# Kernel optimization log

Hardware: AMD Instinct MI355X
Metric: run time of the kernel (lower is better)

## Reference

```python
import jax, jax.numpy as jnp
import numpy as np
import math


def setup_inputs() -> dict:
    key = jax.random.key(0)
    ks = jax.random.split(key, 7)
    d_input, d_state, d_output = 256, 256, 256
    B_, S_ = 8, 4096
    x = jax.random.normal(ks[0], (B_, S_, d_input), dtype=jnp.float32)
    log_lambda_real = jax.random.normal(ks[1], (d_state,), dtype=jnp.float32)
    lambda_imag = jax.random.normal(ks[2], (d_state,), dtype=jnp.float32)
    dt = jnp.clip(0.01 + jax.random.normal(ks[3], (d_state,), dtype=jnp.float32) * 0.01, 0.005, 0.1)
    log_dt = jnp.log(dt)
    B = jax.random.normal(ks[4], (d_state, d_input), dtype=jnp.float32) / d_state ** 0.5
    C_real = jax.random.normal(ks[5], (d_output, d_state), dtype=jnp.float32) / d_state ** 0.5
    C_imag = jax.random.normal(ks[6], (d_output, d_state), dtype=jnp.float32) / d_state ** 0.5
    return {"x": x, "log_lambda_real": log_lambda_real, "lambda_imag": lambda_imag,
            "log_dt": log_dt, "B": B, "C_real": C_real, "C_imag": C_imag}


def reference(x, log_lambda_real, lambda_imag, log_dt, B, C_real, C_imag):
    batch, seq_len, _ = x.shape
    # continuous-time poles and step sizes
    Lambda = -jnp.exp(log_lambda_real) + 1j * lambda_imag            # [N] complex
    dt = jnp.clip(jnp.exp(log_dt), 0.005, 0.1)                       # [N]
    # bilinear discretization
    denom = 1.0 - 0.5 * dt * Lambda                                  # [N] complex
    A_bar = (1.0 + 0.5 * dt * Lambda) / denom                        # [N] complex
    B_bar = (dt / denom)[:, None] * B                                # [N, d_in] complex
    # project input into state space: u[b,s,n] (complex)
    u = jnp.matmul(x, B_bar.real.T) + 1j * jnp.matmul(x, B_bar.imag.T)  # [B,S,N]
    # kernel A^0 .. A^{L-1} via cumprod (faithful to original)
    A_poles = jnp.broadcast_to(A_bar[:, None], (A_bar.shape[0], seq_len))  # [N,S]
    A_cp = jnp.cumprod(A_poles, axis=1)
    A_powers = jnp.concatenate([jnp.ones_like(A_cp[:, :1]), A_cp[:, :-1]], axis=1)  # [N,S]
    # FFT causal convolution
    n_fft = 2 ** math.ceil(math.log2(seq_len * 2 - 1))
    u_t = jnp.swapaxes(u, 1, 2)                                      # [B,N,S]
    u_f = jnp.fft.fft(u_t, n=n_fft, axis=-1)                          # [B,N,F]
    A_f = jnp.fft.fft(A_powers, n=n_fft, axis=-1)                     # [N,F]
    h = jnp.fft.ifft(u_f * A_f[None], n=n_fft, axis=-1)[..., :seq_len]  # [B,N,S]
    h = jnp.swapaxes(h, 1, 2)                                         # [B,S,N]
    # output projection, keep real part
    C_c = C_real + 1j * C_imag                                        # [d_out,N]
    return jnp.matmul(h, C_c.T).real                                  # [B,S,d_out]
```

## Files before the change

### kernel.cpp

```cpp
#include <hip/hip_runtime.h>
#include <hip/hip_bf16.h>

#define BB 8
#define SS 4096
#define NN 256
#define MM (BB*SS)
#define CHUNK 32
#define NCH (SS/CHUNK)

#define WS_FINR 0
#define WS_FINI (BB*NCH*NN)
#define WS_CARR (2*BB*NCH*NN)
#define WS_CARI (3*BB*NCH*NN)
#define WS_FLOATS (4*BB*NCH*NN)
#define WS_V_BYTE  ((size_t)WS_FLOATS * 4)
#define WS_CP_BYTE (WS_V_BYTE + (size_t)MM*NN*2)

typedef __bf16 bf16_t;
typedef bf16_t bf16x8 __attribute__((ext_vector_type(8)));
typedef float  f32x4  __attribute__((ext_vector_type(4)));
typedef unsigned int u32x4 __attribute__((ext_vector_type(4)));

__device__ inline bf16_t f2b(float f) {
    __hip_bfloat16 h = __float2bfloat16(f);
    return __builtin_bit_cast(bf16_t, h);
}
__device__ inline bf16x8 cvt8(f32x4 a, f32x4 b) {
    bf16x8 o;
    o[0]=f2b(a[0]); o[1]=f2b(a[1]); o[2]=f2b(a[2]); o[3]=f2b(a[3]);
    o[4]=f2b(b[0]); o[5]=f2b(b[1]); o[6]=f2b(b[2]); o[7]=f2b(b[3]);
    return o;
}

__device__ inline void ssm_consts(const float* llr, const float* li, const float* ldt,
                                  int n, float& Ar, float& Ai, float& sr, float& si) {
    float lr = -expf(llr[n]);
    float im = li[n];
    float dt = expf(ldt[n]);
    dt = fminf(fmaxf(dt, 0.005f), 0.1f);
    float hr = 0.5f * dt * lr, hi = 0.5f * dt * im;
    float dr = 1.f - hr, di = -hi;
    float inv = 1.f / (dr*dr + di*di);
    Ar = ((1.f + hr)*dr + hi*di) * inv;
    Ai = (hi*dr - (1.f + hr)*di) * inv;
    sr = dt * dr * inv;
    si = -dt * di * inv;
}

__global__ __launch_bounds__(256) void k1(const float* __restrict__ X,
                                          const float* __restrict__ Bw,
                                          const float* __restrict__ llr,
                                          const float* __restrict__ li,
                                          const float* __restrict__ ldt,
                                          __hip_bfloat16* __restrict__ V,
                                          float* __restrict__ finr,
                                          float* __restrict__ fini) {
    __shared__ bf16x8 lds_a[1024];
    __shared__ bf16x8 lds_b[1024];
    __shared__ __align__(16) __hip_bfloat16 vt[128][128];
    int t = threadIdx.x;
    int w = t >> 6, lane = t & 63;
    int q = lane >> 4, r = lane & 15;
    int Nblk = blockIdx.x;
    int Mblk = blockIdx.y;
    int wmt = (w & 1) * 4;
    int wnt = (w >> 1) * 4;
    f32x4 acc[4][4] = {};

    for (int kk = 0; kk < 4; ++kk) {
        int k0 = kk * 64;
        #pragma unroll
        for (int s = 0; s < 4; ++s) {
            int f    = s * 256 + t;
            int tile = f >> 6;
            int ls   = f & 63;
            int mt   = tile >> 1, kb = tile & 1;
            int qq   = ls >> 4, rr = ls & 15;
            int col  = k0 + kb * 32 + qq * 8;
            const f32x4* pa = (const f32x4*)(X  + (size_t)(Mblk*128 + mt*16 + rr) * 256 + col);
            const f32x4* pb = (const f32x4*)(Bw + (size_t)(Nblk*128 + mt*16 + rr) * 256 + col);
            lds_a[f] = cvt8(pa[0], pa[1]);
            lds_b[f] = cvt8(pb[0], pb[1]);
        }
        __syncthreads();
        #pragma unroll
        for (int kb = 0; kb < 2; ++kb) {
            bf16x8 af[4], bfr[4];
            #pragma unroll
            for (int i = 0; i < 4; ++i) {
                af[i]  = lds_a[((wmt + i)*2 + kb)*64 + lane];
                bfr[i] = lds_b[((wnt + i)*2 + kb)*64 + lane];
            }
            #pragma unroll
            for (int mt = 0; mt < 4; ++mt)
                #pragma unroll
                for (int nt = 0; nt < 4; ++nt)
                    acc[mt][nt] = __builtin_amdgcn_mfma_f32_16x16x32_bf16(
                        af[mt], bfr[nt], acc[mt][nt], 0, 0, 0);
        }
        __syncthreads();
    }
    #pragma unroll
    for (int mt = 0; mt < 4; ++mt)
        #pragma unroll
        for (int nt = 0; nt < 4; ++nt)
            #pragma unroll
            for (int reg = 0; reg < 4; ++reg)
                vt[(wmt+mt)*16 + q*4 + reg][(wnt+nt)*16 + r] =
                    __float2bfloat16(acc[mt][nt][reg]);
    __syncthreads();

    int m0 = Mblk * 128;
    #pragma unroll
    for (int jj = 0; jj < 8; ++jj) {
        int s  = t + 256 * jj;
        int rl = s >> 4, cv = s & 15;
        u32x4 val = *(const u32x4*)&vt[rl][cv*8];
        *(u32x4*)(V + (size_t)(m0 + rl) * NN + Nblk*128 + cv*8) = val;
    }
    int n_loc = t & 127, n = Nblk*128 + n_loc;
    float Ar, Ai, sr, si;
    ssm_consts(llr, li, ldt, n, Ar, Ai, sr, si);
    int b = m0 >> 12, cbase = (m0 & 4095) >> 5;
    #pragma unroll
    for (int half = 0; half < 2; ++half) {
        int ch = (t >> 7) + half*2;
        float hr = 0.f, hi = 0.f;
        #pragma unroll 8
        for (int i = 0; i < CHUNK; ++i) {
            float v = __bfloat162float(vt[ch*32 + i][n_loc]);
            float tr = fmaf(Ar, hr, fmaf(-Ai, hi, sr * v));
            float ti = fmaf(Ar, hi, fmaf( Ai, hr, si * v));
            hr = tr; hi = ti;
        }
        int f = (b * NCH + cbase + ch) * NN + n;
        finr[f] = hr; fini[f] = hi;
    }
}

__global__ __launch_bounds__(256) void k2(const float* __restrict__ llr,
                                          const float* __restrict__ li,
                                          const float* __restrict__ ldt,
                                          const float* __restrict__ Cr,
                                          const float* __restrict__ Ci,
                                          float* __restrict__ wsf,
                                          u32x4* __restrict__ Cpack) {
    int t = threadIdx.x;
    if (blockIdx.x < 8) {
        int n = t, b = blockIdx.x;
        float Ar, Ai, sr_, si_;
        ssm_consts(llr, li, ldt, n, Ar, Ai, sr_, si_);
        float pr = Ar, pi = Ai;
        #pragma unroll
        for (int i = 0; i < 5; ++i) { float tt = pr*pr - pi*pi; pi = 2.f*pr*pi; pr = tt; }
        float cr = 0.f, ci = 0.f;
        #pragma unroll 4
        for (int c = 0; c < NCH; ++c) {
            int f = (b * NCH + c) * NN + n;
            wsf[WS_CARR + f] = cr; wsf[WS_CARI + f] = ci;
            float fr = wsf[WS_FINR + f], fi = wsf[WS_FINI + f];
            float tr = fmaf(pr, cr, fmaf(-pi, ci, fr));
            float ti = fmaf(pr, ci, fmaf( pi, cr, fi));
            cr = tr; ci = ti;
        }
    } else {
        int ks = blockIdx.x - 8;
        const float* src = (ks < 8) ? Cr : Ci;
        float sign = (ks < 8) ? 1.f : -1.f;
        #pragma unroll
        for (int jj = 0; jj < 4; ++jj) {
            int s = t + 256 * jj;
            int ot = s >> 6, lane = s & 63;
            int o  = ot*16 + (lane & 15);
            int kb = (ks & 7)*32 + (lane >> 4)*8;
            bf16x8 v;
            #pragma unroll
            for (int e = 0; e < 8; ++e) v[e] = f2b(sign * src[o*256 + kb + e]);
            Cpack[(ks*16 + ot)*64 + lane] = __builtin_bit_cast(u32x4, v);
        }
    }
}

__global__ __launch_bounds__(512) void k3(const __hip_bfloat16* __restrict__ V,
                                          const float* __restrict__ llr,
                                          const float* __restrict__ li,
                                          const float* __restrict__ ldt,
                                          const float* __restrict__ carr,
                                          const float* __restrict__ cari,
                                          const u32x4* __restrict__ Cpack,
                                          float* __restrict__ out) {
    __shared__ __align__(16) char hlds[65536];
    int t = threadIdx.x;
    int m0 = blockIdx.x * 64;
    int b = m0 >> 12, cbase = (m0 & 4095) >> 5;
    {
        int n = t & 255, ch = t >> 8;
        float Ar, Ai, sr, si;
        ssm_consts(llr, li, ldt, n, Ar, Ai, sr, si);
        int f = (b * NCH + cbase + ch) * NN + n;
        float hr = carr[f], hi = cari[f];
        int oct = n >> 3, j = n & 7;
        const __hip_bfloat16* vp = V + (size_t)(m0 + ch*32) * NN + n;
        #pragma unroll 8
        for (int i = 0; i < CHUNK; ++i) {
            float v = __bfloat162float(vp[i * NN]);
            float tr = fmaf(Ar, hr, fmaf(-Ai, hi, sr * v));
            float ti = fmaf(Ar, hi, fmaf( Ai, hr, si * v));
            hr = tr; hi = ti;
            int ml   = ch*32 + i;
            int octp = oct ^ (ml & 31);
            int off  = ((ml*32 + octp) << 4) + (j << 1);
            *(__hip_bfloat16*)(hlds + off)         = __float2bfloat16(hr);
            *(__hip_bfloat16*)(hlds + 32768 + off) = __float2bfloat16(hi);
        }
    }
    __syncthreads();
    int w = t >> 6, lane = t & 63, q = lane >> 4, r = lane & 15;
    f32x4 acc[4][2] = {};
    #pragma unroll
    for (int ks = 0; ks < 16; ++ks) {
        int base = (ks < 8) ? 0 : 32768;
        int kin  = ks & 7;
        bf16x8 af[4];
        #pragma unroll
        for (int mt = 0; mt < 4; ++mt) {
            int ml   = mt*16 + r;
            int octp = (kin*4 + q) ^ (ml & 31);
            af[mt] = *(const bf16x8*)(hlds + base + ((ml*32 + octp) << 4));
        }
        #pragma unroll
        for (int u = 0; u < 2; ++u) {
            bf16x8 bf_ = __builtin_bit_cast(bf16x8, Cpack[(ks*16 + w*2 + u)*64 + lane]);
            #pragma unroll
            for (int mt = 0; mt < 4; ++mt)
                acc[mt][u] = __builtin_amdgcn_mfma_f32_16x16x32_bf16(
                    af[mt], bf_, acc[mt][u], 0, 0, 0);
        }
    }
    #pragma unroll
    for (int mt = 0; mt < 4; ++mt)
        #pragma unroll
        for (int u = 0; u < 2; ++u)
            #pragma unroll
            for (int reg = 0; reg < 4; ++reg)
                out[(size_t)(m0 + mt*16 + q*4 + reg) * NN + (w*2 + u)*16 + r] =
                    acc[mt][u][reg];
}

extern "C" void kernel_launch(void* const* d_in, const int* in_sizes, int n_in,
                              void* d_out, int out_size, void* d_ws, size_t ws_size,
                              hipStream_t stream) {
    const float* x   = (const float*)d_in[0];
    const float* llr = (const float*)d_in[1];
    const float* li  = (const float*)d_in[2];
    const float* ldt = (const float*)d_in[3];
    const float* Bw  = (const float*)d_in[4];
    const float* Cr  = (const float*)d_in[5];
    const float* Ci  = (const float*)d_in[6];

    float* wsf = (float*)d_ws;
    char*  wsb = (char*)d_ws;
    __hip_bfloat16* V = (__hip_bfloat16*)(wsb + WS_V_BYTE);
    u32x4* Cpack      = (u32x4*)(wsb + WS_CP_BYTE);

    k1<<<dim3(2, 256), 256, 0, stream>>>(x, Bw, llr, li, ldt, V,
                                         wsf + WS_FINR, wsf + WS_FINI);
    k2<<<24, 256, 0, stream>>>(llr, li, ldt, Cr, Ci, wsf, Cpack);
    k3<<<512, 512, 0, stream>>>(V, llr, li, ldt,
                                wsf + WS_CARR, wsf + WS_CARI, Cpack, (float*)d_out);
}
```

Baseline: 138.5 us.

## Fuse carry scan into output kernel and store local chunk states from projection kernel

The projection kernel now computes the chunk-local recurrence itself and writes local real and imaginary states (bf16) instead of the projected input. The sequential cross-chunk carry kernel is removed: each output block recomputes its carry by scanning the prior chunk finals and adds the carry times powers of A to the stored local states. The C packing moves into extra blocks of the first kernel, so there are two launches instead of three. This drops a serial kernel and a launch, but doubles the intermediate bf16 traffic, makes later blocks do a longer redundant carry scan (up to 128 steps), and adds bf16 rounding when local and carry states are summed.

Measured after the change: 135.2 us. 2.4% less time.

```diff
diff --git a/kernel.cpp b/kernel.cpp
--- a/kernel.cpp
+++ b/kernel.cpp
@@ -8,13 +8,11 @@
 #define CHUNK 32
 #define NCH (SS/CHUNK)
 
-#define WS_FINR 0
-#define WS_FINI (BB*NCH*NN)
-#define WS_CARR (2*BB*NCH*NN)
-#define WS_CARI (3*BB*NCH*NN)
-#define WS_FLOATS (4*BB*NCH*NN)
-#define WS_V_BYTE  ((size_t)WS_FLOATS * 4)
-#define WS_CP_BYTE (WS_V_BYTE + (size_t)MM*NN*2)
+#define WS_FINR_B  ((size_t)0)
+#define WS_FINI_B  ((size_t)1  << 20)
+#define WS_HLR_B   ((size_t)2  << 20)
+#define WS_HLI_B   ((size_t)18 << 20)
+#define WS_CP_B    ((size_t)34 << 20)
 
 typedef __bf16 bf16_t;
 typedef bf16_t bf16x8 __attribute__((ext_vector_type(8)));
@@ -24,6 +22,21 @@
 __device__ inline bf16_t f2b(float f) {
     __hip_bfloat16 h = __float2bfloat16(f);
     return __builtin_bit_cast(bf16_t, h);
+}
+__device__ inline float b2f(bf16_t v) {
+    unsigned u = (unsigned)__builtin_bit_cast(unsigned short, v) << 16;
+    return __builtin_bit_cast(float, u);
+}
+__device__ inline float b2f_lo(unsigned v) {
+    unsigned u = v << 16; return __builtin_bit_cast(float, u);
+}
+__device__ inline float b2f_hi(unsigned v) {
+    unsigned u = v & 0xffff0000u; return __builtin_bit_cast(float, u);
+}
+__device__ inline unsigned pack2(float lo, float hi) {
+    unsigned a = (unsigned)__builtin_bit_cast(unsigned short, f2b(lo));
+    unsigned b = (unsigned)__builtin_bit_cast(unsigned short, f2b(hi));
+    return a | (b << 16);
 }
 __device__ inline bf16x8 cvt8(f32x4 a, f32x4 b) {
     bf16x8 o;
@@ -47,22 +60,47 @@
     si = -dt * di * inv;
 }
 
-__global__ __launch_bounds__(256) void k1(const float* __restrict__ X,
-                                          const float* __restrict__ Bw,
-                                          const float* __restrict__ llr,
-                                          const float* __restrict__ li,
-                                          const float* __restrict__ ldt,
-                                          __hip_bfloat16* __restrict__ V,
-                                          float* __restrict__ finr,
-                                          float* __restrict__ fini) {
-    __shared__ bf16x8 lds_a[1024];
-    __shared__ bf16x8 lds_b[1024];
-    __shared__ __align__(16) __hip_bfloat16 vt[128][128];
+__global__ __launch_bounds__(256, 2) void k1(const float* __restrict__ X,
+                                             const float* __restrict__ Bw,
+                                             const float* __restrict__ llr,
+                                             const float* __restrict__ li,
+                                             const float* __restrict__ ldt,
+                                             const float* __restrict__ Cr,
+                                             const float* __restrict__ Ci,
+                                             __hip_bfloat16* __restrict__ HLR,
+                                             __hip_bfloat16* __restrict__ HLI,
+                                             float* __restrict__ finr,
+                                             float* __restrict__ fini,
+                                             u32x4* __restrict__ Cpack) {
+    __shared__ __align__(16) char smem[65536];
+    bf16x8* lds_a = (bf16x8*)smem;
+    bf16x8* lds_b = (bf16x8*)(smem + 16384);
+    __hip_bfloat16 (*vt)[128]  = (__hip_bfloat16(*)[128])(smem + 32768);
+    __hip_bfloat16 (*hit)[128] = (__hip_bfloat16(*)[128])smem;
+
     int t = threadIdx.x;
+    int bid = blockIdx.x;
+    if (bid >= 512) {
+        int ks = bid - 512;
+        const float* src = (ks < 8) ? Cr : Ci;
+        float sign = (ks < 8) ? 1.f : -1.f;
+        #pragma unroll
+        for (int jj = 0; jj < 4; ++jj) {
+            int s = t + 256 * jj;
+            int ot = s >> 6, lane = s & 63;
+            int o  = ot*16 + (lane & 15);
+            int kb = (ks & 7)*32 + (lane >> 4)*8;
+            bf16x8 v;
+            #pragma unroll
+            for (int e = 0; e < 8; ++e) v[e] = f2b(sign * src[o*256 + kb + e]);
+            Cpack[(ks*16 + ot)*64 + lane] = __builtin_bit_cast(u32x4, v);
+        }
+        return;
+    }
+
     int w = t >> 6, lane = t & 63;
     int q = lane >> 4, r = lane & 15;
-    int Nblk = blockIdx.x;
-    int Mblk = blockIdx.y;
+    int Nblk = bid & 1, Mblk = bid >> 1;
     int wmt = (w & 1) * 4;
     int wnt = (w >> 1) * 4;
     f32x4 acc[4][4] = {};
@@ -111,108 +149,109 @@
     __syncthreads();
 
     int m0 = Mblk * 128;
+    int b = m0 >> 12, cbase = (m0 & 4095) >> 5;
+    {
+        int p = t & 63, ch = t >> 6;
+        int n0 = Nblk*128 + p*2;
+        float Ar0,Ai0,sr0,si0, Ar1,Ai1,sr1,si1;
+        ssm_consts(llr, li, ldt, n0,   Ar0, Ai0, sr0, si0);
+        ssm_consts(llr, li, ldt, n0+1, Ar1, Ai1, sr1, si1);
+        float hr0=0.f, hi0=0.f, hr1=0.f, hi1=0.f;
+        #pragma unroll 8
+        for (int i = 0; i < CHUNK; ++i) {
+            int row = ch*32 + i;
+            unsigned vv = *(unsigned*)&vt[row][p*2];
+            float v0 = b2f_lo(vv), v1 = b2f_hi(vv);
+            float t0r = fmaf(Ar0, hr0, fmaf(-Ai0, hi0, sr0 * v0));
+            float t0i = fmaf(Ar0, hi0, fmaf( Ai0, hr0, si0 * v0));
+            float t1r = fmaf(Ar1, hr1, fmaf(-Ai1, hi1, sr1 * v1));
+            float t1i = fmaf(Ar1, hi1, fmaf( Ai1, hr1, si1 * v1));
+            hr0=t0r; hi0=t0i; hr1=t1r; hi1=t1i;
+            *(unsigned*)&vt[row][p*2]  = pack2(hr0, hr1);
+            *(unsigned*)&hit[row][p*2] = pack2(hi0, hi1);
+        }
+        int f = (b * NCH + cbase + ch) * NN + n0;
+        finr[f] = hr0; finr[f+1] = hr1;
+        fini[f] = hi0; fini[f+1] = hi1;
+    }
+    __syncthreads();
     #pragma unroll
     for (int jj = 0; jj < 8; ++jj) {
         int s  = t + 256 * jj;
         int rl = s >> 4, cv = s & 15;
-        u32x4 val = *(const u32x4*)&vt[rl][cv*8];
-        *(u32x4*)(V + (size_t)(m0 + rl) * NN + Nblk*128 + cv*8) = val;
-    }
-    int n_loc = t & 127, n = Nblk*128 + n_loc;
-    float Ar, Ai, sr, si;
-    ssm_consts(llr, li, ldt, n, Ar, Ai, sr, si);
-    int b = m0 >> 12, cbase = (m0 & 4095) >> 5;
-    #pragma unroll
-    for (int half = 0; half < 2; ++half) {
-        int ch = (t >> 7) + half*2;
-        float hr = 0.f, hi = 0.f;
-        #pragma unroll 8
-        for (int i = 0; i < CHUNK; ++i) {
-            float v = __bfloat162float(vt[ch*32 + i][n_loc]);
-            float tr = fmaf(Ar, hr, fmaf(-Ai, hi, sr * v));
-            float ti = fmaf(Ar, hi, fmaf( Ai, hr, si * v));
-            hr = tr; hi = ti;
-        }
-        int f = (b * NCH + cbase + ch) * NN + n;
-        finr[f] = hr; fini[f] = hi;
-    }
-}
-
-__global__ __launch_bounds__(256) void k2(const float* __restrict__ llr,
-                                          const float* __restrict__ li,
-                                          const float* __restrict__ ldt,
-                                          const float* __restrict__ Cr,
-                                          const float* __restrict__ Ci,
-                                          float* __restrict__ wsf,
-                                          u32x4* __restrict__ Cpack) {
-    int t = threadIdx.x;
-    if (blockIdx.x < 8) {
-        int n = t, b = blockIdx.x;
-        float Ar, Ai, sr_, si_;
-        ssm_consts(llr, li, ldt, n, Ar, Ai, sr_, si_);
-        float pr = Ar, pi = Ai;
-        #pragma unroll
-        for (int i = 0; i < 5; ++i) { float tt = pr*pr - pi*pi; pi = 2.f*pr*pi; pr = tt; }
-        float cr = 0.f, ci = 0.f;
-        #pragma unroll 4
-        for (int c = 0; c < NCH; ++c) {
-            int f = (b * NCH + c) * NN + n;
-            wsf[WS_CARR + f] = cr; wsf[WS_CARI + f] = ci;
-            float fr = wsf[WS_FINR + f], fi = wsf[WS_FINI + f];
-            float tr = fmaf(pr, cr, fmaf(-pi, ci, fr));
-            float ti = fmaf(pr, ci, fmaf( pi, cr, fi));
-            cr = tr; ci = ti;
-        }
-    } else {
-        int ks = blockIdx.x - 8;
-        const float* src = (ks < 8) ? Cr : Ci;
-        float sign = (ks < 8) ? 1.f : -1.f;
-        #pragma unroll
-        for (int jj = 0; jj < 4; ++jj) {
-            int s = t + 256 * jj;
-            int ot = s >> 6, lane = s & 63;
-            int o  = ot*16 + (lane & 15);
-            int kb = (ks & 7)*32 + (lane >> 4)*8;
-            bf16x8 v;
-            #pragma unroll
-            for (int e = 0; e < 8; ++e) v[e] = f2b(sign * src[o*256 + kb + e]);
-            Cpack[(ks*16 + ot)*64 + lane] = __builtin_bit_cast(u32x4, v);
-        }
-    }
-}
-
-__global__ __launch_bounds__(512) void k3(const __hip_bfloat16* __restrict__ V,
-                                          const float* __restrict__ llr,
-                                          const float* __restrict__ li,
-                                          const float* __restrict__ ldt,
-                                          const float* __restrict__ carr,
-                                          const float* __restrict__ cari,
-                                          const u32x4* __restrict__ Cpack,
-                                          float* __restrict__ out) {
+        *(u32x4*)(HLR + (size_t)(m0 + rl) * NN + Nblk*128 + cv*8) = *(const u32x4*)&vt[rl][cv*8];
+        *(u32x4*)(HLI + (size_t)(m0 + rl) * NN + Nblk*128 + cv*8) = *(const u32x4*)&hit[rl][cv*8];
+    }
+}
+
+__global__ __launch_bounds__(512, 4) void k3(const __hip_bfloat16* __restrict__ HLR,
+                                             const __hip_bfloat16* __restrict__ HLI,
+                                             const float* __restrict__ finr,
+                                             const float* __restrict__ fini,
+                                             const float* __restrict__ llr,
+                                             const float* __restrict__ li,
+                                             const float* __restrict__ ldt,
+                                             const u32x4* __restrict__ Cpack,
+                                             float* __restrict__ out) {
     __shared__ __align__(16) char hlds[65536];
     int t = threadIdx.x;
     int m0 = blockIdx.x * 64;
     int b = m0 >> 12, cbase = (m0 & 4095) >> 5;
+
     {
-        int n = t & 255, ch = t >> 8;
-        float Ar, Ai, sr, si;
-        ssm_consts(llr, li, ldt, n, Ar, Ai, sr, si);
-        int f = (b * NCH + cbase + ch) * NN + n;
-        float hr = carr[f], hi = cari[f];
-        int oct = n >> 3, j = n & 7;
-        const __hip_bfloat16* vp = V + (size_t)(m0 + ch*32) * NN + n;
+        int n = t & 255, d = t >> 8;
+        float Ar, Ai, sr_, si_;
+        ssm_consts(llr, li, ldt, n, Ar, Ai, sr_, si_);
+        float Pr = Ar, Pi = Ai;
+        #pragma unroll
+        for (int i = 0; i < 5; ++i) { float tt = Pr*Pr - Pi*Pi; Pi = 2.f*Pr*Pi; Pr = tt; }
+        float cr = 0.f, ci = 0.f;
+        int ce = cbase + d;
+        #pragma unroll 4
+        for (int j = 0; j < ce; ++j) {
+            int f = (b * NCH + j) * NN + n;
+            float fr = finr[f], fi = fini[f];
+            float tr = fmaf(Pr, cr, fmaf(-Pi, ci, fr));
+            float ti = fmaf(Pr, ci, fmaf( Pi, cr, fi));
+            cr = tr; ci = ti;
+        }
+        float gr = Ar*cr - Ai*ci;
+        float gi = Ar*ci + Ai*cr;
+        int oct = n >> 3, j2 = (n & 7) * 2;
         #pragma unroll 8
         for (int i = 0; i < CHUNK; ++i) {
-            float v = __bfloat162float(vp[i * NN]);
-            float tr = fmaf(Ar, hr, fmaf(-Ai, hi, sr * v));
-            float ti = fmaf(Ar, hi, fmaf( Ai, hr, si * v));
-            hr = tr; hi = ti;
-            int ml   = ch*32 + i;
-            int octp = oct ^ (ml & 31);
-            int off  = ((ml*32 + octp) << 4) + (j << 1);
-            *(__hip_bfloat16*)(hlds + off)         = __float2bfloat16(hr);
-            *(__hip_bfloat16*)(hlds + 32768 + off) = __float2bfloat16(hi);
-        }
+            int row  = d*32 + i;
+            int octp = oct ^ (row & 31);
+            int off  = ((row*32 + octp) << 4) + j2;
+            *(__hip_bfloat16*)(hlds + off)         = __float2bfloat16(gr);
+            *(__hip_bfloat16*)(hlds + 32768 + off) = __float2bfloat16(gi);
+            float tg = Ar*gr - Ai*gi;
+            gi = fmaf(Ar, gi, Ai*gr);
+            gr = tg;
+        }
+    }
+    __syncthreads();
+    #pragma unroll
+    for (int jj = 0; jj < 4; ++jj) {
+        int s = t + 512*jj;
+        int row = s >> 5, oct = s & 31;
+        int octp = oct ^ (row & 31);
+        char* ptr_r = hlds + ((row*32 + octp) << 4);
+        char* ptr_i = ptr_r + 32768;
+        u32x4 hru = *(const u32x4*)(HLR + (size_t)(m0 + row) * NN + oct*8);
+        u32x4 hiu = *(const u32x4*)(HLI + (size_t)(m0 + row) * NN + oct*8);
+        bf16x8 hl_r = __builtin_bit_cast(bf16x8, hru);
+        bf16x8 hl_i = __builtin_bit_cast(bf16x8, hiu);
+        bf16x8 g_r = *(const bf16x8*)ptr_r;
+        bf16x8 g_i = *(const bf16x8*)ptr_i;
+        bf16x8 o_r, o_i;
+        #pragma unroll
+        for (int e = 0; e < 8; ++e) {
+            o_r[e] = f2b(b2f(hl_r[e]) + b2f(g_r[e]));
+            o_i[e] = f2b(b2f(hl_i[e]) + b2f(g_i[e]));
+        }
+        *(bf16x8*)ptr_r = o_r;
+        *(bf16x8*)ptr_i = o_i;
     }
     __syncthreads();
     int w = t >> 6, lane = t & 63, q = lane >> 4, r = lane & 15;
@@ -258,14 +297,15 @@
     const float* Cr  = (const float*)d_in[5];
     const float* Ci  = (const float*)d_in[6];
 
-    float* wsf = (float*)d_ws;
-    char*  wsb = (char*)d_ws;
-    __hip_bfloat16* V = (__hip_bfloat16*)(wsb + WS_V_BYTE);
-    u32x4* Cpack      = (u32x4*)(wsb + WS_CP_BYTE);
-
-    k1<<<dim3(2, 256), 256, 0, stream>>>(x, Bw, llr, li, ldt, V,
-                                         wsf + WS_FINR, wsf + WS_FINI);
-    k2<<<24, 256, 0, stream>>>(llr, li, ldt, Cr, Ci, wsf, Cpack);
-    k3<<<512, 512, 0, stream>>>(V, llr, li, ldt,
-                                wsf + WS_CARR, wsf + WS_CARI, Cpack, (float*)d_out);
-}
+    char* wsb = (char*)d_ws;
+    float* finr = (float*)(wsb + WS_FINR_B);
+    float* fini = (float*)(wsb + WS_FINI_B);
+    __hip_bfloat16* HLR = (__hip_bfloat16*)(wsb + WS_HLR_B);
+    __hip_bfloat16* HLI = (__hip_bfloat16*)(wsb + WS_HLI_B);
+    u32x4* Cpack        = (u32x4*)(wsb + WS_CP_B);
+
+    k1<<<528, 256, 0, stream>>>(x, Bw, llr, li, ldt, Cr, Ci,
+                                HLR, HLI, finr, fini, Cpack);
+    k3<<<512, 512, 0, stream>>>(HLR, HLI, finr, fini, llr, li, ldt,
+                                Cpack, (float*)d_out);
+}
```

## Merge carry scan into output kernel and fuse C packing into projection kernel

Applied to the files above, without the earlier changes.

Reduces three launches to two: the projection kernel now covers all 256 state columns per 64-row block and also packs the C matrices, and the output kernel recomputes its chunk carry by scanning prior chunk finals itself instead of relying on a separate serial scan kernel. V is staged into LDS with coalesced vector loads before the intra-chunk recurrence. This removes a serial, low-occupancy scan kernel and a launch boundary, at the cost of redundant, imbalanced carry recomputation (up to 127 steps) in later blocks.

Result: no change. 136.7 us (-1.3%).

```diff
diff --git a/kernel.cpp b/kernel.cpp
--- a/kernel.cpp
+++ b/kernel.cpp
@@ -8,13 +8,10 @@
 #define CHUNK 32
 #define NCH (SS/CHUNK)
 
-#define WS_FINR 0
-#define WS_FINI (BB*NCH*NN)
-#define WS_CARR (2*BB*NCH*NN)
-#define WS_CARI (3*BB*NCH*NN)
-#define WS_FLOATS (4*BB*NCH*NN)
-#define WS_V_BYTE  ((size_t)WS_FLOATS * 4)
-#define WS_CP_BYTE (WS_V_BYTE + (size_t)MM*NN*2)
+#define WS_FINR_B  ((size_t)0)
+#define WS_FINI_B  ((size_t)1 << 20)
+#define WS_CP_B    ((size_t)2 << 20)
+#define WS_V_B     ((size_t)3 << 20)
 
 typedef __bf16 bf16_t;
 typedef bf16_t bf16x8 __attribute__((ext_vector_type(8)));
@@ -24,6 +21,10 @@
 __device__ inline bf16_t f2b(float f) {
     __hip_bfloat16 h = __float2bfloat16(f);
     return __builtin_bit_cast(bf16_t, h);
+}
+__device__ inline float b2f(bf16_t v) {
+    unsigned u = (unsigned)__builtin_bit_cast(unsigned short, v) << 16;
+    return __builtin_bit_cast(float, u);
 }
 __device__ inline bf16x8 cvt8(f32x4 a, f32x4 b) {
     bf16x8 o;
@@ -47,176 +48,178 @@
     si = -dt * di * inv;
 }
 
-__global__ __launch_bounds__(256) void k1(const float* __restrict__ X,
-                                          const float* __restrict__ Bw,
-                                          const float* __restrict__ llr,
-                                          const float* __restrict__ li,
-                                          const float* __restrict__ ldt,
-                                          __hip_bfloat16* __restrict__ V,
-                                          float* __restrict__ finr,
-                                          float* __restrict__ fini) {
-    __shared__ bf16x8 lds_a[1024];
-    __shared__ bf16x8 lds_b[1024];
-    __shared__ __align__(16) __hip_bfloat16 vt[128][128];
+__device__ inline int swz(int row, int oct) {
+    return ((row*32 + (oct ^ (row & 31))) << 4);
+}
+
+__global__ __launch_bounds__(512, 4) void kA(
+        const float* __restrict__ X,   const float* __restrict__ Bw,
+        const float* __restrict__ llr, const float* __restrict__ li,
+        const float* __restrict__ ldt, const float* __restrict__ Cr,
+        const float* __restrict__ Ci,  __hip_bfloat16* __restrict__ V,
+        float* __restrict__ finr,      float* __restrict__ fini,
+        u32x4* __restrict__ Cpack) {
+    __shared__ __align__(16) char smem[40960];
+    bf16x8* ldsA = (bf16x8*)smem;
+    bf16x8* ldsB = (bf16x8*)(smem + 8192);
+
     int t = threadIdx.x;
-    int w = t >> 6, lane = t & 63;
-    int q = lane >> 4, r = lane & 15;
-    int Nblk = blockIdx.x;
-    int Mblk = blockIdx.y;
-    int wmt = (w & 1) * 4;
-    int wnt = (w >> 1) * 4;
-    f32x4 acc[4][4] = {};
-
+    int bid = blockIdx.x;
+    int w = t >> 6, lane = t & 63, q = lane >> 4, r = lane & 15;
+
+    if (bid >= 512) {
+        int ks = bid - 512;
+        const float* src = (ks < 8) ? Cr : Ci;
+        float sign = (ks < 8) ? 1.f : -1.f;
+        #pragma unroll
+        for (int jj = 0; jj < 2; ++jj) {
+            int s = t + 512 * jj;
+            int ot = s >> 6, ln = s & 63;
+            int o  = ot*16 + (ln & 15);
+            int kb = (ks & 7)*32 + (ln >> 4)*8;
+            bf16x8 v;
+            #pragma unroll
+            for (int e = 0; e < 8; ++e) v[e] = f2b(sign * src[o*256 + kb + e]);
+            Cpack[(ks*16 + ot)*64 + ln] = __builtin_bit_cast(u32x4, v);
+        }
+        return;
+    }
+
+    int m0 = bid * 64;
+    int mt2 = (w & 1) * 2;
+    int nt4 = (w >> 1) * 4;
+    f32x4 acc1[2][4] = {};
     for (int kk = 0; kk < 4; ++kk) {
         int k0 = kk * 64;
         #pragma unroll
-        for (int s = 0; s < 4; ++s) {
-            int f    = s * 256 + t;
-            int tile = f >> 6;
-            int ls   = f & 63;
-            int mt   = tile >> 1, kb = tile & 1;
-            int qq   = ls >> 4, rr = ls & 15;
-            int col  = k0 + kb * 32 + qq * 8;
-            const f32x4* pa = (const f32x4*)(X  + (size_t)(Mblk*128 + mt*16 + rr) * 256 + col);
-            const f32x4* pb = (const f32x4*)(Bw + (size_t)(Nblk*128 + mt*16 + rr) * 256 + col);
-            lds_a[f] = cvt8(pa[0], pa[1]);
-            lds_b[f] = cvt8(pb[0], pb[1]);
+        for (int j = 0; j < 5; ++j) {
+            int s = t + 512 * j;
+            if (s < 512) {
+                int tile = s >> 6, ls = s & 63;
+                int mt = tile >> 1, kb = tile & 1;
+                int col = k0 + kb*32 + (ls >> 4)*8;
+                const f32x4* p = (const f32x4*)(X + (size_t)(m0 + mt*16 + (ls & 15)) * 256 + col);
+                ldsA[s] = cvt8(p[0], p[1]);
+            } else {
+                int s2 = s - 512;
+                int tile = s2 >> 6, ls = s2 & 63;
+                int nt = tile >> 1, kb = tile & 1;
+                int col = k0 + kb*32 + (ls >> 4)*8;
+                const f32x4* p = (const f32x4*)(Bw + (size_t)(nt*16 + (ls & 15)) * 256 + col);
+                ldsB[s2] = cvt8(p[0], p[1]);
+            }
         }
         __syncthreads();
         #pragma unroll
         for (int kb = 0; kb < 2; ++kb) {
-            bf16x8 af[4], bfr[4];
-            #pragma unroll
-            for (int i = 0; i < 4; ++i) {
-                af[i]  = lds_a[((wmt + i)*2 + kb)*64 + lane];
-                bfr[i] = lds_b[((wnt + i)*2 + kb)*64 + lane];
+            bf16x8 af[2], bf_[4];
+            #pragma unroll
+            for (int i = 0; i < 2; ++i) af[i]  = ldsA[((mt2 + i)*2 + kb)*64 + lane];
+            #pragma unroll
+            for (int i = 0; i < 4; ++i) bf_[i] = ldsB[((nt4 + i)*2 + kb)*64 + lane];
+            #pragma unroll
+            for (int mi = 0; mi < 2; ++mi)
+                #pragma unroll
+                for (int ni = 0; ni < 4; ++ni)
+                    acc1[mi][ni] = __builtin_amdgcn_mfma_f32_16x16x32_bf16(
+                        af[mi], bf_[ni], acc1[mi][ni], 0, 0, 0);
+        }
+        __syncthreads();
+    }
+    #pragma unroll
+    for (int mi = 0; mi < 2; ++mi)
+        #pragma unroll
+        for (int ni = 0; ni < 4; ++ni)
+            #pragma unroll
+            for (int reg = 0; reg < 4; ++reg) {
+                int m = (mt2 + mi)*16 + q*4 + reg;
+                int n = (nt4 + ni)*16 + r;
+                *(bf16_t*)(smem + swz(m, n >> 3) + (n & 7)*2) =
+                    f2b(acc1[mi][ni][reg]);
             }
-            #pragma unroll
-            for (int mt = 0; mt < 4; ++mt)
-                #pragma unroll
-                for (int nt = 0; nt < 4; ++nt)
-                    acc[mt][nt] = __builtin_amdgcn_mfma_f32_16x16x32_bf16(
-                        af[mt], bfr[nt], acc[mt][nt], 0, 0, 0);
-        }
-        __syncthreads();
-    }
-    #pragma unroll
-    for (int mt = 0; mt < 4; ++mt)
-        #pragma unroll
-        for (int nt = 0; nt < 4; ++nt)
-            #pragma unroll
-            for (int reg = 0; reg < 4; ++reg)
-                vt[(wmt+mt)*16 + q*4 + reg][(wnt+nt)*16 + r] =
-                    __float2bfloat16(acc[mt][nt][reg]);
     __syncthreads();
 
-    int m0 = Mblk * 128;
-    #pragma unroll
-    for (int jj = 0; jj < 8; ++jj) {
-        int s  = t + 256 * jj;
-        int rl = s >> 4, cv = s & 15;
-        u32x4 val = *(const u32x4*)&vt[rl][cv*8];
-        *(u32x4*)(V + (size_t)(m0 + rl) * NN + Nblk*128 + cv*8) = val;
-    }
-    int n_loc = t & 127, n = Nblk*128 + n_loc;
-    float Ar, Ai, sr, si;
-    ssm_consts(llr, li, ldt, n, Ar, Ai, sr, si);
-    int b = m0 >> 12, cbase = (m0 & 4095) >> 5;
-    #pragma unroll
-    for (int half = 0; half < 2; ++half) {
-        int ch = (t >> 7) + half*2;
+    #pragma unroll
+    for (int j = 0; j < 4; ++j) {
+        int s = t + 512*j;
+        int row = s >> 5, oct = s & 31;
+        *(u32x4*)(V + (size_t)(m0 + row) * NN + oct*8) =
+            *(const u32x4*)(smem + swz(row, oct));
+    }
+    {
+        int n_s = t & 255, d_s = t >> 8;
+        int b = bid >> 6, cbase = (bid & 63) * 2;
+        float Ar, Ai, sr, si;
+        ssm_consts(llr, li, ldt, n_s, Ar, Ai, sr, si);
+        int oct = n_s >> 3, j2 = (n_s & 7) * 2;
         float hr = 0.f, hi = 0.f;
         #pragma unroll 8
         for (int i = 0; i < CHUNK; ++i) {
-            float v = __bfloat162float(vt[ch*32 + i][n_loc]);
+            float v = b2f(*(const bf16_t*)(smem + swz(d_s*32 + i, oct) + j2));
             float tr = fmaf(Ar, hr, fmaf(-Ai, hi, sr * v));
             float ti = fmaf(Ar, hi, fmaf( Ai, hr, si * v));
             hr = tr; hi = ti;
         }
-        int f = (b * NCH + cbase + ch) * NN + n;
+        int f = (b * NCH + cbase + d_s) * NN + n_s;
         finr[f] = hr; fini[f] = hi;
     }
 }
 
-__global__ __launch_bounds__(256) void k2(const float* __restrict__ llr,
-                                          const float* __restrict__ li,
-                                          const float* __restrict__ ldt,
-                                          const float* __restrict__ Cr,
-                                          const float* __restrict__ Ci,
-                                          float* __restrict__ wsf,
-                                          u32x4* __restrict__ Cpack) {
+__global__ __launch_bounds__(512, 4) void kB(
+        const __hip_bfloat16* __restrict__ V,
+        const float* __restrict__ finr, const float* __restrict__ fini,
+        const float* __restrict__ llr,  const float* __restrict__ li,
+        const float* __restrict__ ldt,  const u32x4* __restrict__ Cpack,
+        float* __restrict__ out) {
+    __shared__ __align__(16) char smem[65536];
     int t = threadIdx.x;
-    if (blockIdx.x < 8) {
-        int n = t, b = blockIdx.x;
-        float Ar, Ai, sr_, si_;
-        ssm_consts(llr, li, ldt, n, Ar, Ai, sr_, si_);
-        float pr = Ar, pi = Ai;
-        #pragma unroll
-        for (int i = 0; i < 5; ++i) { float tt = pr*pr - pi*pi; pi = 2.f*pr*pi; pr = tt; }
+    int bid = blockIdx.x;
+    int m0 = bid * 64;
+    int b = bid >> 6, cbase = (bid & 63) * 2;
+
+    #pragma unroll
+    for (int j = 0; j < 4; ++j) {
+        int s = t + 512*j;
+        int row = s >> 5, oct = s & 31;
+        *(u32x4*)(smem + swz(row, oct)) =
+            *(const u32x4*)(V + (size_t)(m0 + row) * NN + oct*8);
+    }
+    __syncthreads();
+
+    {
+        int n_s = t & 255, d_s = t >> 8;
+        float Ar, Ai, sr, si;
+        ssm_consts(llr, li, ldt, n_s, Ar, Ai, sr, si);
+        float Pr = Ar, Pi = Ai;
+        #pragma unroll
+        for (int i = 0; i < 5; ++i) { float tt = Pr*Pr - Pi*Pi; Pi = 2.f*Pr*Pi; Pr = tt; }
         float cr = 0.f, ci = 0.f;
+        int ce = cbase + d_s;
         #pragma unroll 4
-        for (int c = 0; c < NCH; ++c) {
-            int f = (b * NCH + c) * NN + n;
-            wsf[WS_CARR + f] = cr; wsf[WS_CARI + f] = ci;
-            float fr = wsf[WS_FINR + f], fi = wsf[WS_FINI + f];
-            float tr = fmaf(pr, cr, fmaf(-pi, ci, fr));
-            float ti = fmaf(pr, ci, fmaf( pi, cr, fi));
+        for (int j = 0; j < ce; ++j) {
+            int f = (b * NCH + j) * NN + n_s;
+            float fr = finr[f], fi = fini[f];
+            float tr = fmaf(Pr, cr, fmaf(-Pi, ci, fr));
+            float ti = fmaf(Pr, ci, fmaf( Pi, cr, fi));
             cr = tr; ci = ti;
         }
-    } else {
-        int ks = blockIdx.x - 8;
-        const float* src = (ks < 8) ? Cr : Ci;
-        float sign = (ks < 8) ? 1.f : -1.f;
-        #pragma unroll
-        for (int jj = 0; jj < 4; ++jj) {
-            int s = t + 256 * jj;
-            int ot = s >> 6, lane = s & 63;
-            int o  = ot*16 + (lane & 15);
-            int kb = (ks & 7)*32 + (lane >> 4)*8;
-            bf16x8 v;
-            #pragma unroll
-            for (int e = 0; e < 8; ++e) v[e] = f2b(sign * src[o*256 + kb + e]);
-            Cpack[(ks*16 + ot)*64 + lane] = __builtin_bit_cast(u32x4, v);
-        }
-    }
-}
-
-__global__ __launch_bounds__(512) void k3(const __hip_bfloat16* __restrict__ V,
-                                          const float* __restrict__ llr,
-                                          const float* __restrict__ li,
-                                          const float* __restrict__ ldt,
-                                          const float* __restrict__ carr,
-                                          const float* __restrict__ cari,
-                                          const u32x4* __restrict__ Cpack,
-                                          float* __restrict__ out) {
-    __shared__ __align__(16) char hlds[65536];
-    int t = threadIdx.x;
-    int m0 = blockIdx.x * 64;
-    int b = m0 >> 12, cbase = (m0 & 4095) >> 5;
-    {
-        int n = t & 255, ch = t >> 8;
-        float Ar, Ai, sr, si;
-        ssm_consts(llr, li, ldt, n, Ar, Ai, sr, si);
-        int f = (b * NCH + cbase + ch) * NN + n;
-        float hr = carr[f], hi = cari[f];
-        int oct = n >> 3, j = n & 7;
-        const __hip_bfloat16* vp = V + (size_t)(m0 + ch*32) * NN + n;
+        int oct = n_s >> 3, j2 = (n_s & 7) * 2;
+        float hr = cr, hi = ci;
         #pragma unroll 8
         for (int i = 0; i < CHUNK; ++i) {
-            float v = __bfloat162float(vp[i * NN]);
+            int off = swz(d_s*32 + i, oct) + j2;
+            float v = b2f(*(const bf16_t*)(smem + off));
             float tr = fmaf(Ar, hr, fmaf(-Ai, hi, sr * v));
             float ti = fmaf(Ar, hi, fmaf( Ai, hr, si * v));
             hr = tr; hi = ti;
-            int ml   = ch*32 + i;
-            int octp = oct ^ (ml & 31);
-            int off  = ((ml*32 + octp) << 4) + (j << 1);
-            *(__hip_bfloat16*)(hlds + off)         = __float2bfloat16(hr);
-            *(__hip_bfloat16*)(hlds + 32768 + off) = __float2bfloat16(hi);
+            *(bf16_t*)(smem + off)         = f2b(hr);
+            *(bf16_t*)(smem + 32768 + off) = f2b(hi);
         }
     }
     __syncthreads();
+
     int w = t >> 6, lane = t & 63, q = lane >> 4, r = lane & 15;
-    f32x4 acc[4][2] = {};
+    f32x4 acc2[4][2] = {};
     #pragma unroll
     for (int ks = 0; ks < 16; ++ks) {
         int base = (ks < 8) ? 0 : 32768;
@@ -224,17 +227,17 @@
         bf16x8 af[4];
         #pragma unroll
         for (int mt = 0; mt < 4; ++mt) {
-            int ml   = mt*16 + r;
+            int ml = mt*16 + r;
             int octp = (kin*4 + q) ^ (ml & 31);
-            af[mt] = *(const bf16x8*)(hlds + base + ((ml*32 + octp) << 4));
+            af[mt] = *(const bf16x8*)(smem + base + ((ml*32 + octp) << 4));
         }
         #pragma unroll
         for (int u = 0; u < 2; ++u) {
             bf16x8 bf_ = __builtin_bit_cast(bf16x8, Cpack[(ks*16 + w*2 + u)*64 + lane]);
             #pragma unroll
             for (int mt = 0; mt < 4; ++mt)
-                acc[mt][u] = __builtin_amdgcn_mfma_f32_16x16x32_bf16(
-                    af[mt], bf_, acc[mt][u], 0, 0, 0);
+                acc2[mt][u] = __builtin_amdgcn_mfma_f32_16x16x32_bf16(
+                    af[mt], bf_, acc2[mt][u], 0, 0, 0);
         }
     }
     #pragma unroll
@@ -244,7 +247,7 @@
             #pragma unroll
             for (int reg = 0; reg < 4; ++reg)
                 out[(size_t)(m0 + mt*16 + q*4 + reg) * NN + (w*2 + u)*16 + r] =
-                    acc[mt][u][reg];
+                    acc2[mt][u][reg];
 }
 
 extern "C" void kernel_launch(void* const* d_in, const int* in_sizes, int n_in,
@@ -258,14 +261,12 @@
     const float* Cr  = (const float*)d_in[5];
     const float* Ci  = (const float*)d_in[6];
 
-    float* wsf = (float*)d_ws;
-    char*  wsb = (char*)d_ws;
-    __hip_bfloat16* V = (__hip_bfloat16*)(wsb + WS_V_BYTE);
-    u32x4* Cpack      = (u32x4*)(wsb + WS_CP_BYTE);
-
-    k1<<<dim3(2, 256), 256, 0, stream>>>(x, Bw, llr, li, ldt, V,
-                                         wsf + WS_FINR, wsf + WS_FINI);
-    k2<<<24, 256, 0, stream>>>(llr, li, ldt, Cr, Ci, wsf, Cpack);
-    k3<<<512, 512, 0, stream>>>(V, llr, li, ldt,
-                                wsf + WS_CARR, wsf + WS_CARI, Cpack, (float*)d_out);
-}
+    char* wsb = (char*)d_ws;
+    float* finr  = (float*)(wsb + WS_FINR_B);
+    float* fini  = (float*)(wsb + WS_FINI_B);
+    u32x4* Cpack = (u32x4*)(wsb + WS_CP_B);
+    __hip_bfloat16* V = (__hip_bfloat16*)(wsb + WS_V_B);
+
+    kA<<<528, 512, 0, stream>>>(x, Bw, llr, li, ldt, Cr, Ci, V, finr, fini, Cpack);
+    kB<<<512, 512, 0, stream>>>(V, finr, fini, llr, li, ldt, Cpack, (float*)d_out);
+}
```
